# Performance work log

Hardware: AMD Instinct MI355X
Metric: run time of the kernel (lower is better)

## Reference

```python
import jax, jax.numpy as jnp
import numpy as np

B, S, IN, HID, NH, HD, R, WIN, TK = 2, 2048, 64, 512, 8, 64, 64, 5, 16
C1, C2, C3 = 171, 171, 170  # hidden_dim split across 3 conv branches (512 = 171+171+170)


def _conv(xc, w, b, pad):
    y = jax.lax.conv_general_dilated(xc, w, window_strides=(1,), padding=[(pad, pad)],
                                     dimension_numbers=('NCH', 'OIH', 'NCH'))
    return jax.nn.relu(y + b[None, :, None])


def setup_inputs():
    key = jax.random.key(0)
    ks = jax.random.split(key, 22)
    p = lambda k, sh: jax.random.normal(k, sh, jnp.float32) * 0.05
    return {
        'x': jax.random.normal(ks[0], (B, S, IN), jnp.float32),
        'conv1_w': p(ks[1], (C1, IN, 3)), 'conv1_b': p(ks[2], (C1,)),
        'conv2_w': p(ks[3], (C2, IN, 5)), 'conv2_b': p(ks[4], (C2,)),
        'conv3_w': p(ks[5], (C3, IN, 7)), 'conv3_b': p(ks[6], (C3,)),
        'Wq': p(ks[7], (HID, HID)), 'bq': p(ks[8], (HID,)),
        'Wk': p(ks[9], (HID, HID)), 'bk': p(ks[10], (HID,)),
        'Wv': p(ks[11], (HID, HID)), 'bv': p(ks[12], (HID,)),
        'Wkp': p(ks[13], (R, HD)), 'bkp': p(ks[14], (R,)),
        'Wvp': p(ks[15], (R, HD)), 'bvp': p(ks[16], (R,)),
        'Wo': p(ks[17], (HID, HID)), 'bo': p(ks[18], (HID,)),
        'ln_g': jnp.ones((HID,), jnp.float32), 'ln_b': jnp.zeros((HID,), jnp.float32),
    }


def reference(x, conv1_w, conv1_b, conv2_w, conv2_b, conv3_w, conv3_b,
              Wq, bq, Wk, bk, Wv, bv, Wkp, bkp, Wvp, bvp, Wo, bo, ln_g, ln_b):
    # multi-scale conv front-end
    xc = x.transpose(0, 2, 1)  # [B, IN, S]
    h = jnp.concatenate([_conv(xc, conv1_w, conv1_b, 1),
                         _conv(xc, conv2_w, conv2_b, 2),
                         _conv(xc, conv3_w, conv3_b, 3)], axis=1).transpose(0, 2, 1)  # [B,S,HID]

    def heads(W_, b_):
        return (h @ W_.T + b_).reshape(B, S, NH, HD).transpose(0, 2, 1, 3)  # [B,NH,S,HD]

    Q, K, V = heads(Wq, bq), heads(Wk, bk), heads(Wv, bv)
    Kp = K @ Wkp.T + bkp  # [B,NH,S,R]
    Vp = V @ Wvp.T + bvp

    # local sliding-window attention; -inf masking reproduces the per-t boundary slicing
    hw = WIN // 2
    idx = jnp.arange(S)[:, None] + jnp.arange(-hw, hw + 1)[None, :]
    valid = (idx >= 0) & (idx < S)
    idxc = jnp.clip(idx, 0, S - 1)
    Kw = K[:, :, idxc, :]
    Vw = V[:, :, idxc, :]
    ls = jnp.einsum('bhsd,bhswd->bhsw', Q, Kw) / jnp.sqrt(jnp.float32(HD))
    ls = jnp.where(valid[None, None], ls, -jnp.inf)
    local = jnp.einsum('bhsw,bhswd->bhsd', jax.nn.softmax(ls, axis=-1), Vw)

    # top-k low-rank global attention (HD == R required by original einsum)
    gs = jnp.einsum('bhqd,bhkd->bhqk', Q, Kp) / jnp.sqrt(jnp.float32(R))  # [B,NH,S,S]
    tv, ti = jax.lax.top_k(gs, TK)
    tw = jax.nn.softmax(tv, axis=-1)  # [B,NH,S,TK]
    bi = jnp.arange(B)[:, None, None, None]
    hi = jnp.arange(NH)[None, :, None, None]
    topV = Vp[bi, hi, ti]  # [B,NH,S,TK,R]
    sp = jnp.einsum('bhqk,bhqkr->bhqr', tw, topV)
    sp = sp @ Wvp.T + bvp  # extra value_proj applied to sparse output, as in original

    out = ((local + sp) * 0.5).transpose(0, 2, 1, 3).reshape(B, S, HID)
    out = out @ Wo.T + bo
    res = out + h
    mu = res.mean(-1, keepdims=True)
    var = ((res - mu) ** 2).mean(-1, keepdims=True)
    return (res - mu) / jnp.sqrt(var + 1e-5) * ln_g + ln_b
```

## Files before the change

kernel.cpp:

```cpp
#include <hip/hip_runtime.h>
#include <hip/hip_bf16.h>

#define BB 2
#define SS 2048
#define INC 64
#define HIDN 512
#define NHH 8
#define HDD 64
#define SP 2054

typedef __attribute__((ext_vector_type(8))) short bf16x8;
typedef __attribute__((ext_vector_type(4))) float f32x4;

__device__ __forceinline__ short f2bf(float f) {
  union { __hip_bfloat16 h; short s; } u;
  u.h = __float2bfloat16(f);
  return u.s;
}
__device__ __forceinline__ float bf2f(short s) {
  return __uint_as_float(((unsigned)(unsigned short)s) << 16);
}


__global__ __launch_bounds__(256) void prep_kernel(
    const float* __restrict__ x, const float* __restrict__ w1,
    const float* __restrict__ b1, const float* __restrict__ w2,
    const float* __restrict__ b2, const float* __restrict__ w3,
    const float* __restrict__ b3, const float* __restrict__ bq,
    const float* __restrict__ bk_, const float* __restrict__ bv_,
    const float* __restrict__ Wkp, const float* __restrict__ Wvp,
    const float* __restrict__ bvp, float* __restrict__ ball,
    short* __restrict__ Wkpbf, short* __restrict__ W2bf,
    float* __restrict__ cvec, short* __restrict__ xbfp,
    short* __restrict__ Wcbf, float* __restrict__ bcat) {
  int i0 = blockIdx.x * 256 + threadIdx.x;
  int stride = gridDim.x * 256;
  for (int g = i0; g < BB * SP * 8; g += stride) {
    int row = g >> 3, c0 = (g & 7) << 3;
    int b = row / SP, pr = row - b * SP;
    int sg = pr - 3;
    bf16x8 v;
    if (sg >= 0 && sg < SS) {
      const float* src = x + ((size_t)(b * SS + sg) << 6) + c0;
      float4 f0 = *(const float4*)src;
      float4 f1 = *(const float4*)(src + 4);
      v[0] = f2bf(f0.x); v[1] = f2bf(f0.y); v[2] = f2bf(f0.z); v[3] = f2bf(f0.w);
      v[4] = f2bf(f1.x); v[5] = f2bf(f1.y); v[6] = f2bf(f1.z); v[7] = f2bf(f1.w);
    } else {
#pragma unroll
      for (int e = 0; e < 8; e++) v[e] = 0;
    }
    *(bf16x8*)(xbfp + ((size_t)row << 6) + c0) = v;
  }
  for (int g = i0; g < 28672; g += stride) {
    int c = g / 56;
    int rem = g - c * 56;
    int k = rem << 3;
    int t = k >> 6;
    int ci0 = k & 63;
    bf16x8 v;
#pragma unroll
    for (int e = 0; e < 8; e++) {
      int ci = ci0 + e;
      float val = 0.f;
      if (c < 171) {
        int kk = t - 2;
        if (kk >= 0 && kk < 3) val = w1[(c * 64 + ci) * 3 + kk];
      } else if (c < 342) {
        int kk = t - 1;
        if (kk >= 0 && kk < 5) val = w2[((c - 171) * 64 + ci) * 5 + kk];
      } else {
        val = w3[((c - 342) * 64 + ci) * 7 + t];
      }
      v[e] = f2bf(val);
    }
    size_t off = (size_t)(c >> 6) * 28672 + (size_t)(k >> 5) * 2048 +
                 (size_t)((c & 63) >> 4) * 512 +
                 ((((k & 31) >> 3) * 16 + (c & 15)) << 3);
    *(bf16x8*)(Wcbf + off) = v;
  }
  for (int idx = i0; idx < 4096; idx += stride) {
    Wkpbf[idx] = f2bf(Wkp[idx]);
    int j = idx >> 6, d = idx & 63;
    float s = 0.f;
#pragma unroll 8
    for (int i = 0; i < 64; i++) s += Wvp[j * 64 + i] * Wvp[i * 64 + d];
    W2bf[idx] = f2bf(s);
  }
  if (i0 < 1536) {
    float v;
    if (i0 < 512)       v = bq[i0];
    else if (i0 < 1024) v = bk_[i0 - 512];
    else                v = bv_[i0 - 1024];
    ball[i0] = v;
  }
  if (i0 < 512) {
    float v;
    if (i0 < 171)      v = b1[i0];
    else if (i0 < 342) v = b2[i0 - 171];
    else               v = b3[i0 - 342];
    bcat[i0] = v;
  }
  if (i0 < 64) {
    float s = bvp[i0];
#pragma unroll 8
    for (int i = 0; i < 64; i++) s += bvp[i] * Wvp[i0 * 64 + i];
    cvec[i0] = s;
  }
}

__global__ __launch_bounds__(256, 4) void gemm_conv_fused(
    const short* __restrict__ xbfp, const short* __restrict__ Wcbf,
    const float* __restrict__ bcat, short* __restrict__ hbf,
    short* __restrict__ hAf, const float* __restrict__ Wq,
    const float* __restrict__ Wk_, const float* __restrict__ Wv_,
    const float* __restrict__ Wo, short* __restrict__ Wallbf,
    short* __restrict__ Wobf) {
  int blk = blockIdx.x;
  int tid = threadIdx.x;
  if (blk >= 256) {
    int i0 = (blk - 256) * 256 + tid;
    if (i0 < 98304) {
      int n = i0 >> 6;
      int k = (i0 & 63) << 3;
      const float* src;
      if (n < 512)       src = Wq  + (size_t)n * 512 + k;
      else if (n < 1024) src = Wk_ + (size_t)(n - 512) * 512 + k;
      else               src = Wv_ + (size_t)(n - 1024) * 512 + k;
      float4 f0 = *(const float4*)src;
      float4 f1 = *(const float4*)(src + 4);
      bf16x8 v;
      v[0] = f2bf(f0.x); v[1] = f2bf(f0.y); v[2] = f2bf(f0.z); v[3] = f2bf(f0.w);
      v[4] = f2bf(f1.x); v[5] = f2bf(f1.y); v[6] = f2bf(f1.z); v[7] = f2bf(f1.w);
      size_t off = (size_t)(n >> 6) * 32768 + (size_t)(k >> 5) * 2048 +
                   (size_t)((n & 63) >> 4) * 512 +
                   ((((k & 31) >> 3) * 16 + (n & 15)) << 3);
      *(bf16x8*)(Wallbf + off) = v;
    } else {
      int g = i0 - 98304;
      int n = g >> 6;
      int k = (g & 63) << 3;
      const float* src = Wo + (size_t)n * 512 + k;
      float4 f0 = *(const float4*)src;
      float4 f1 = *(const float4*)(src + 4);
      bf16x8 v;
      v[0] = f2bf(f0.x); v[1] = f2bf(f0.y); v[2] = f2bf(f0.z); v[3] = f2bf(f0.w);
      v[4] = f2bf(f1.x); v[5] = f2bf(f1.y); v[6] = f2bf(f1.z); v[7] = f2bf(f1.w);
      size_t off = (size_t)(n >> 6) * 32768 + (size_t)(k >> 5) * 2048 +
                   (size_t)((n & 63) >> 4) * 512 +
                   ((((k & 31) >> 3) * 16 + (n & 15)) << 3);
      *(bf16x8*)(Wobf + off) = v;
    }
    return;
  }
  int m0 = (blk >> 3) * 128;
  int n0 = (blk & 7) * 64;
  int wvv = tid >> 6, lane = tid & 63;
  int quad = lane >> 4, l16 = lane & 15;
  int mw = m0 + wvv * 32;
  int r0 = mw + l16, r1 = r0 + 16;
  int b0 = r0 >> 11, s0 = r0 & 2047;
  int b1 = r1 >> 11, s1 = r1 & 2047;
  const short* ap0 = xbfp + (size_t)(b0 * SP + s0) * 64 + quad * 8;
  const short* ap1 = xbfp + (size_t)(b1 * SP + s1) * 64 + quad * 8;
  const short* bp = Wcbf + (size_t)(n0 >> 6) * 28672 + lane * 8;
  f32x4 acc[2][4] = {};
  bf16x8 cA0 = *(const bf16x8*)ap0;
  bf16x8 cA1 = *(const bf16x8*)ap1;
  bf16x8 cB0 = *(const bf16x8*)(bp + 0 * 512);
  bf16x8 cB1 = *(const bf16x8*)(bp + 1 * 512);
  bf16x8 cB2 = *(const bf16x8*)(bp + 2 * 512);
  bf16x8 cB3 = *(const bf16x8*)(bp + 3 * 512);
#pragma unroll 2
  for (int ks = 0; ks < 14; ks++) {
    int kn = (ks + 1 < 14 ? ks + 1 : 13);
    int offa = kn * 32;
    int offb = kn * 2048;
    bf16x8 nA0 = *(const bf16x8*)(ap0 + offa);
    bf16x8 nA1 = *(const bf16x8*)(ap1 + offa);
    bf16x8 nB0 = *(const bf16x8*)(bp + offb + 0 * 512);
    bf16x8 nB1 = *(const bf16x8*)(bp + offb + 1 * 512);
    bf16x8 nB2 = *(const bf16x8*)(bp + offb + 2 * 512);
    bf16x8 nB3 = *(const bf16x8*)(bp + offb + 3 * 512);
    acc[0][0] = __builtin_amdgcn_mfma_f32_16x16x32_bf16(cA0, cB0, acc[0][0], 0, 0, 0);
    acc[1][0] = __builtin_amdgcn_mfma_f32_16x16x32_bf16(cA1, cB0, acc[1][0], 0, 0, 0);
    acc[0][1] = __builtin_amdgcn_mfma_f32_16x16x32_bf16(cA0, cB1, acc[0][1], 0, 0, 0);
    acc[1][1] = __builtin_amdgcn_mfma_f32_16x16x32_bf16(cA1, cB1, acc[1][1], 0, 0, 0);
    acc[0][2] = __builtin_amdgcn_mfma_f32_16x16x32_bf16(cA0, cB2, acc[0][2], 0, 0, 0);
    acc[1][2] = __builtin_amdgcn_mfma_f32_16x16x32_bf16(cA1, cB2, acc[1][2], 0, 0, 0);
    acc[0][3] = __builtin_amdgcn_mfma_f32_16x16x32_bf16(cA0, cB3, acc[0][3], 0, 0, 0);
    acc[1][3] = __builtin_amdgcn_mfma_f32_16x16x32_bf16(cA1, cB3, acc[1][3], 0, 0, 0);
    cA0 = nA0; cA1 = nA1;
    cB0 = nB0; cB1 = nB1; cB2 = nB2; cB3 = nB3;
  }
#pragma unroll
  for (int mt = 0; mt < 2; mt++) {
#pragma unroll
    for (int r = 0; r < 4; r++) {
      int m = mw + mt * 16 + quad * 4 + r;
      size_t abase = (size_t)(m >> 4) * 8192;
      int m15 = m & 15;
#pragma unroll
      for (int t = 0; t < 4; t++) {
        int n = n0 + t * 16 + l16;
        float v = fmaxf(acc[mt][t][r] + bcat[n], 0.f);
        short val = f2bf(v);
        hbf[(size_t)m * 512 + n] = val;
        hAf[abase + (size_t)(n >> 5) * 512 +
            ((((n & 31) >> 3) * 16 + m15) << 3) + (n & 7)] = val;
      }
    }
  }
}

__global__ __launch_bounds__(256, 4) void gemm_qkv(
    const short* __restrict__ hAf, const short* __restrict__ Wbf,
    const float* __restrict__ bias, short* __restrict__ Qh,
    short* __restrict__ Kh, short* __restrict__ Vh) {
  int m0 = blockIdx.x * 128;
  int n0 = blockIdx.y * 64;
  int tid = threadIdx.x;
  int wvv = tid >> 6, lane = tid & 63;
  int quad = lane >> 4, l16 = lane & 15;
  int mw = m0 + wvv * 32;
  const short* ap0 = hAf + (size_t)(mw >> 4) * 8192 + lane * 8;
  const short* ap1 = ap0 + 8192;
  const short* bp = Wbf + (size_t)(n0 >> 6) * 32768 + lane * 8;
  f32x4 acc[2][4] = {};
  bf16x8 cA0 = *(const bf16x8*)ap0;
  bf16x8 cA1 = *(const bf16x8*)ap1;
  bf16x8 cB0 = *(const bf16x8*)(bp + 0 * 512);
  bf16x8 cB1 = *(const bf16x8*)(bp + 1 * 512);
  bf16x8 cB2 = *(const bf16x8*)(bp + 2 * 512);
  bf16x8 cB3 = *(const bf16x8*)(bp + 3 * 512);
#pragma unroll 2
  for (int ks = 0; ks < 16; ks++) {
    int kn = (ks + 1 < 16 ? ks + 1 : 15);
    int offab = kn * 512;
    int offb = kn * 2048;
    bf16x8 nA0 = *(const bf16x8*)(ap0 + offab);
    bf16x8 nA1 = *(const bf16x8*)(ap1 + offab);
    bf16x8 nB0 = *(const bf16x8*)(bp + offb + 0 * 512);
    bf16x8 nB1 = *(const bf16x8*)(bp + offb + 1 * 512);
    bf16x8 nB2 = *(const bf16x8*)(bp + offb + 2 * 512);
    bf16x8 nB3 = *(const bf16x8*)(bp + offb + 3 * 512);
    acc[0][0] = __builtin_amdgcn_mfma_f32_16x16x32_bf16(cA0, cB0, acc[0][0], 0, 0, 0);
    acc[1][0] = __builtin_amdgcn_mfma_f32_16x16x32_bf16(cA1, cB0, acc[1][0], 0, 0, 0);
    acc[0][1] = __builtin_amdgcn_mfma_f32_16x16x32_bf16(cA0, cB1, acc[0][1], 0, 0, 0);
    acc[1][1] = __builtin_amdgcn_mfma_f32_16x16x32_bf16(cA1, cB1, acc[1][1], 0, 0, 0);
    acc[0][2] = __builtin_amdgcn_mfma_f32_16x16x32_bf16(cA0, cB2, acc[0][2], 0, 0, 0);
    acc[1][2] = __builtin_amdgcn_mfma_f32_16x16x32_bf16(cA1, cB2, acc[1][2], 0, 0, 0);
    acc[0][3] = __builtin_amdgcn_mfma_f32_16x16x32_bf16(cA0, cB3, acc[0][3], 0, 0, 0);
    acc[1][3] = __builtin_amdgcn_mfma_f32_16x16x32_bf16(cA1, cB3, acc[1][3], 0, 0, 0);
    cA0 = nA0; cA1 = nA1;
    cB0 = nB0; cB1 = nB1; cB2 = nB2; cB3 = nB3;
  }
  int which = n0 >> 9;
  int head = (n0 >> 6) & 7;
  short* dst = which == 0 ? Qh : (which == 1 ? Kh : Vh);
  float scale = which == 0 ? 0.125f : 1.0f;
#pragma unroll
  for (int mt = 0; mt < 2; mt++) {
#pragma unroll
    for (int r = 0; r < 4; r++) {
      int m = mw + mt * 16 + quad * 4 + r;
      int bb = m >> 11, s = m & 2047;
      size_t rowoff = ((size_t)(bb * 8 + head) * 2048 + s) * 64;
#pragma unroll
      for (int t = 0; t < 4; t++) {
        int hd = t * 16 + l16;
        float v = acc[mt][t][r] + bias[n0 + hd];
        dst[rowoff + hd] = f2bf(v * scale);
      }
    }
  }
}

__global__ __launch_bounds__(256, 4) void kpvp_local_kernel(
    const short* __restrict__ Kh, const short* __restrict__ Vh,
    const short* __restrict__ Wkpbf, const float* __restrict__ bkp,
    const short* __restrict__ W2bf, const float* __restrict__ cvec,
    short* __restrict__ Kfrag, float* __restrict__ Vpp,
    const short* __restrict__ Qh, float* __restrict__ ctxl) {
  int tid = threadIdx.x;
  __shared__ float Sloc[4][2][16][17];
  __shared__ float wloc[4][16][8];
  if (blockIdx.x < 256) {
    int m0 = blockIdx.x * 128;
    int wvv = tid >> 6, lane = tid & 63;
    int quad = lane >> 4, l16 = lane & 15;
    int mw = m0 + wvv * 32;
    {
      const short* ap0 = Kh + (size_t)(mw + l16) * 64 + quad * 8;
      const short* ap1 = ap0 + 16 * 64;
      const short* bp = Wkpbf + l16 * 64 + quad * 8;
      bf16x8 A00 = *(const bf16x8*)ap0, A01 = *(const bf16x8*)(ap0 + 32);
      bf16x8 A10 = *(const bf16x8*)ap1, A11 = *(const bf16x8*)(ap1 + 32);
      f32x4 acc[2][4] = {};
#pragma unroll
      for (int t = 0; t < 4; t++) {
        bf16x8 B0 = *(const bf16x8*)(bp + t * 16 * 64);
        bf16x8 B1 = *(const bf16x8*)(bp + t * 16 * 64 + 32);
        acc[0][t] = __builtin_amdgcn_mfma_f32_16x16x32_bf16(A00, B0, acc[0][t], 0, 0, 0);
        acc[0][t] = __builtin_amdgcn_mfma_f32_16x16x32_bf16(A01, B1, acc[0][t], 0, 0, 0);
        acc[1][t] = __builtin_amdgcn_mfma_f32_16x16x32_bf16(A10, B0, acc[1][t], 0, 0, 0);
        acc[1][t] = __builtin_amdgcn_mfma_f32_16x16x32_bf16(A11, B1, acc[1][t], 0, 0, 0);
      }
#pragma unroll
      for (int mt = 0; mt < 2; mt++)
#pragma unroll
        for (int r = 0; r < 4; r++) {
          int m = mw + mt * 16 + quad * 4 + r;
          int m15 = m & 15;
          size_t gbase = (size_t)(m >> 4) * 1024;
#pragma unroll
          for (int t = 0; t < 4; t++) {
            int n = t * 16 + l16;
            short val = f2bf(acc[mt][t][r] + bkp[n]);
            Kfrag[gbase + (size_t)(n >> 5) * 512 +
                  ((((n & 31) >> 3) * 16 + m15) << 3) + (n & 7)] = val;
          }
        }
    }
    {
      const short* ap0 = Vh + (size_t)(mw + l16) * 64 + quad * 8;
      const short* ap1 = ap0 + 16 * 64;
      const short* bp = W2bf + l16 * 64 + quad * 8;
      bf16x8 A00 = *(const bf16x8*)ap0, A01 = *(const bf16x8*)(ap0 + 32);
      bf16x8 A10 = *(const bf16x8*)ap1, A11 = *(const bf16x8*)(ap1 + 32);
      f32x4 acc[2][4] = {};
#pragma unroll
      for (int t = 0; t < 4; t++) {
        bf16x8 B0 = *(const bf16x8*)(bp + t * 16 * 64);
        bf16x8 B1 = *(const bf16x8*)(bp + t * 16 * 64 + 32);
        acc[0][t] = __builtin_amdgcn_mfma_f32_16x16x32_bf16(A00, B0, acc[0][t], 0, 0, 0);
        acc[0][t] = __builtin_amdgcn_mfma_f32_16x16x32_bf16(A01, B1, acc[0][t], 0, 0, 0);
        acc[1][t] = __builtin_amdgcn_mfma_f32_16x16x32_bf16(A10, B0, acc[1][t], 0, 0, 0);
        acc[1][t] = __builtin_amdgcn_mfma_f32_16x16x32_bf16(A11, B1, acc[1][t], 0, 0, 0);
      }
#pragma unroll
      for (int mt = 0; mt < 2; mt++)
#pragma unroll
        for (int r = 0; r < 4; r++) {
          int m = mw + mt * 16 + quad * 4 + r;
#pragma unroll
          for (int t = 0; t < 4; t++) {
            int n = t * 16 + l16;
            Vpp[(size_t)m * 64 + n] = acc[mt][t][r] + cvec[n];
          }
        }
    }
    return;
  }
  int wv = tid >> 6;
  int tile = (blockIdx.x - 256) * 4 + wv;
  int bh = tile >> 7;
  int q0 = (tile & 127) * 16;
  int lane = tid & 63;
  int quad = lane >> 4, l16 = lane & 15;

  const short* qbase = Qh + (size_t)(bh * 2048 + q0 + l16) * 64 + quad * 8;
  bf16x8 a0 = *(const bf16x8*)qbase;
  bf16x8 a1 = *(const bf16x8*)(qbase + 32);

  int k0a = min(max(q0 - 2 + l16, 0), 2047);
  int k1a = min(q0 + 6 + l16, 2047);
  const short* kb0 = Kh + (size_t)(bh * 2048 + k0a) * 64 + quad * 8;
  const short* kb1 = Kh + (size_t)(bh * 2048 + k1a) * 64 + quad * 8;
  bf16x8 B00 = *(const bf16x8*)kb0;
  bf16x8 B01 = *(const bf16x8*)(kb0 + 32);
  bf16x8 B10 = *(const bf16x8*)kb1;
  bf16x8 B11 = *(const bf16x8*)(kb1 + 32);
  f32x4 C0 = {0.f, 0.f, 0.f, 0.f};
  f32x4 C1 = {0.f, 0.f, 0.f, 0.f};
  C0 = __builtin_amdgcn_mfma_f32_16x16x32_bf16(a0, B00, C0, 0, 0, 0);
  C0 = __builtin_amdgcn_mfma_f32_16x16x32_bf16(a1, B01, C0, 0, 0, 0);
  C1 = __builtin_amdgcn_mfma_f32_16x16x32_bf16(a0, B10, C1, 0, 0, 0);
  C1 = __builtin_amdgcn_mfma_f32_16x16x32_bf16(a1, B11, C1, 0, 0, 0);
#pragma unroll
  for (int r = 0; r < 4; r++) {
    Sloc[wv][0][quad * 4 + r][l16] = C0[r];
    Sloc[wv][1][quad * 4 + r][l16] = C1[r];
  }
  __builtin_amdgcn_wave_barrier();
  if (lane < 16) {
    int q = lane;
    float sc[5];
    bool ok[5];
#pragma unroll
    for (int j = 0; j < 5; j++) {
      int offq = q + j - 2;
      int sg = q0 + offq;
      ok[j] = (sg >= 0 && sg < SS);
      int t = offq <= 13 ? 0 : 1;
      int col = t ? offq - 6 : offq + 2;
      sc[j] = ok[j] ? Sloc[wv][t][q][col] : -3.0e38f;
    }
    float m = -3.0e38f;
#pragma unroll
    for (int j = 0; j < 5; j++) m = fmaxf(m, sc[j]);
    float e[5], l = 0.f;
#pragma unroll
    for (int j = 0; j < 5; j++) {
      e[j] = ok[j] ? __expf(sc[j] - m) : 0.f;
      l += e[j];
    }
    float inv = 1.f / l;
#pragma unroll
    for (int j = 0; j < 5; j++) wloc[wv][q][j] = e[j] * inv;
  }
  __builtin_amdgcn_wave_barrier();
  {
    int q = lane >> 2, jb = (lane & 3) * 16;
    int s = q0 + q;
    float acc[16] = {};
#pragma unroll
    for (int j = 0; j < 5; j++) {
      int sg = s + j - 2;
      if (sg >= 0 && sg < SS) {
        float w = wloc[wv][q][j];
        const short* vr = Vh + (size_t)(bh * 2048 + sg) * 64 + jb;
#pragma unroll
        for (int u = 0; u < 16; u += 4) {
          short4 v4 = *(const short4*)(vr + u);
          acc[u + 0] += w * bf2f(v4.x);
          acc[u + 1] += w * bf2f(v4.y);
          acc[u + 2] += w * bf2f(v4.z);
          acc[u + 3] += w * bf2f(v4.w);
        }
      }
    }
    float* orow = ctxl + (size_t)(bh * 2048 + s) * 64 + jb;
#pragma unroll
    for (int u = 0; u < 16; u += 4)
      *(float4*)(orow + u) =
          make_float4(acc[u], acc[u + 1], acc[u + 2], acc[u + 3]);
  }
}

__global__ __launch_bounds__(256, 4) void global_attn(
    const short* __restrict__ Qh, const short* __restrict__ Kfrag,
    const float* __restrict__ Vpp, const float* __restrict__ ctxl,
    short* __restrict__ ctxcb) {
  int tid = threadIdx.x;
  int wv = tid >> 6;
  int lane = tid & 63;
  int quad = lane >> 4, l16 = lane & 15;
  int tb = wv >> 1;
  int half = wv & 1;
  int p = blockIdx.x;
  int bh = (p & 7) * 2 + ((p >> 3) & 1);
  int seg = p >> 4;
  int tile = seg * 2 + tb;
  int q0 = tile * 16;

  __shared__ unsigned swl[4][16][17];
  __shared__ float twl[2][16][17];
  __shared__ int   txl[2][16][17];

  const short* qbase = Qh + (size_t)(bh * 2048 + q0 + l16) * 64 + quad * 8;
  bf16x8 a0 = *(const bf16x8*)qbase;
  bf16x8 a1 = *(const bf16x8*)(qbase + 32);

  const short* kf =
      Kfrag + (size_t)bh * (128 * 1024) + (size_t)half * (64 * 1024) + lane * 8;

  unsigned er[4][8];
#pragma unroll
  for (int a = 0; a < 4; a++)
#pragma unroll
    for (int j = 0; j < 8; j++) er[a][j] = 0u;

  auto insert8 = [&](unsigned (&e)[8], unsigned cand) {
    unsigned n0, n1, n2, n3, n4, n5, n6, n7;
    asm("v_max_u32 %0, %1, %2" : "=v"(n0) : "v"(e[0]), "v"(cand));
    asm("v_med3_u32 %0, %1, %2, %3" : "=v"(n1) : "v"(e[0]), "v"(e[1]), "v"(cand));
    asm("v_med3_u32 %0, %1, %2, %3" : "=v"(n2) : "v"(e[1]), "v"(e[2]), "v"(cand));
    asm("v_med3_u32 %0, %1, %2, %3" : "=v"(n3) : "v"(e[2]), "v"(e[3]), "v"(cand));
    asm("v_med3_u32 %0, %1, %2, %3" : "=v"(n4) : "v"(e[3]), "v"(e[4]), "v"(cand));
    asm("v_med3_u32 %0, %1, %2, %3" : "=v"(n5) : "v"(e[4]), "v"(e[5]), "v"(cand));
    asm("v_med3_u32 %0, %1, %2, %3" : "=v"(n6) : "v"(e[5]), "v"(e[6]), "v"(cand));
    asm("v_med3_u32 %0, %1, %2, %3" : "=v"(n7) : "v"(e[6]), "v"(e[7]), "v"(cand));
    e[0] = n0; e[1] = n1; e[2] = n2; e[3] = n3;
    e[4] = n4; e[5] = n5; e[6] = n6; e[7] = n7;
  };
  auto mkcand = [&](float s, int idxr) -> unsigned {
    unsigned u = __float_as_uint(s);
    u ^= ((unsigned)((int)u >> 31)) | 0x80000000u;
    return (u & 0xFFFFF800u) | (unsigned)idxr;
  };

  int idxb = 2047 - half * 1024 - l16;
#pragma unroll 4
  for (int g = 0; g < 64; g++) {
    bf16x8 B00 = *(const bf16x8*)(kf + g * 1024);
    bf16x8 B01 = *(const bf16x8*)(kf + g * 1024 + 512);
    f32x4 C0 = {0.f, 0.f, 0.f, 0.f};
    C0 = __builtin_amdgcn_mfma_f32_16x16x32_bf16(a0, B00, C0, 0, 0, 0);
    C0 = __builtin_amdgcn_mfma_f32_16x16x32_bf16(a1, B01, C0, 0, 0, 0);
    int idxr = idxb - (g << 4);
    insert8(er[0], mkcand(C0[0], idxr));
    insert8(er[1], mkcand(C0[1], idxr));
    insert8(er[2], mkcand(C0[2], idxr));
    insert8(er[3], mkcand(C0[3], idxr));
  }

  {
    unsigned sw[4] = {0u, 0u, 0u, 0u};
#pragma unroll
    for (int t = 0; t < 16; t++) {
#pragma unroll
      for (int a = 0; a < 4; a++) {
        unsigned w = er[a][0];
#pragma unroll
        for (int mm = 1; mm <= 8; mm <<= 1) {
          unsigned o = (unsigned)__shfl_xor((int)w, mm);
          w = w > o ? w : o;
        }
        bool pop = (er[a][0] == w);
#pragma unroll
        for (int j = 0; j < 7; j++) er[a][j] = pop ? er[a][j + 1] : er[a][j];
        er[a][7] = pop ? 0u : er[a][7];
        if (l16 == t) sw[a] = w;
      }
    }
#pragma unroll
    for (int a = 0; a < 4; a++) swl[wv][quad * 4 + a][l16] = sw[a];
  }
  __syncthreads();

  if (tid < 32) {
    int tb2 = tid >> 4, q = tid & 15;
    const unsigned* A = swl[tb2 * 2][q];
    const unsigned* Bv = swl[tb2 * 2 + 1][q];
    auto decode = [&](unsigned w) -> float {
      unsigned wb = w & 0xFFFFF800u;
      unsigned uu = (w & 0x80000000u) ? (wb ^ 0x80000000u) : ~wb;
      return (w == 0u) ? -1.0e30f : __uint_as_float(uu);
    };
    unsigned h0 = A[0], h1 = Bv[0];
    float mval = decode(h0 > h1 ? h0 : h1);
    float lsum = 0.f;
    float ev[16];
    int ki[16];
#pragma unroll
    for (int i = 0; i < 16; i++) {
      unsigned wa = A[i], wb2 = Bv[15 - i];
      unsigned w = wa > wb2 ? wa : wb2;
      float sv = decode(w);
      float ex = __expf(sv - mval);
      lsum += ex;
      ev[i] = ex;
      ki[i] = 2047 - (int)(w & 0x7FFu);
    }
    float inv = 1.f / lsum;
#pragma unroll
    for (int i = 0; i < 16; i++) {
      twl[tb2][q][i] = ev[i] * inv;
      txl[tb2][q][i] = ki[i];
    }
  }
  __syncthreads();

  {
    int tb2 = tid >> 7;
    int r = tid & 127;
    int q = r >> 3, d0 = (r & 7) * 8;
    int tile2 = seg * 2 + tb2;
    int q02 = tile2 * 16;
    int b = bh >> 3, hh = bh & 7;
    const float* vball = Vpp + (size_t)bh * (2048 * 64) + d0;
    float acc[8];
#pragma unroll
    for (int u = 0; u < 8; u++) acc[u] = 0.f;
#pragma unroll 4
    for (int j = 0; j < 16; j++) {
      float w = twl[tb2][q][j];
      const float* vr = vball + (size_t)txl[tb2][q][j] * 64;
      float4 v0 = *(const float4*)vr;
      float4 v1 = *(const float4*)(vr + 4);
      acc[0] += w * v0.x; acc[1] += w * v0.y;
      acc[2] += w * v0.z; acc[3] += w * v0.w;
      acc[4] += w * v1.x; acc[5] += w * v1.y;
      acc[6] += w * v1.z; acc[7] += w * v1.w;
    }
    int s = q02 + q;
    const float* lrow = ctxl + (size_t)(bh * 2048 + s) * 64 + d0;
    int M = b * 2048 + s;
    int k = hh * 64 + d0;
    size_t aoff = (size_t)(M >> 4) * 8192 + (size_t)(k >> 5) * 512 +
                  ((((k & 31) >> 3) * 16 + (M & 15)) << 3);
    float4 lv0 = *(const float4*)lrow;
    float4 lv1 = *(const float4*)(lrow + 4);
    short4 o0, o1;
    o0.x = f2bf(0.5f * (lv0.x + acc[0]));
    o0.y = f2bf(0.5f * (lv0.y + acc[1]));
    o0.z = f2bf(0.5f * (lv0.z + acc[2]));
    o0.w = f2bf(0.5f * (lv0.w + acc[3]));
    o1.x = f2bf(0.5f * (lv1.x + acc[4]));
    o1.y = f2bf(0.5f * (lv1.y + acc[5]));
    o1.z = f2bf(0.5f * (lv1.z + acc[6]));
    o1.w = f2bf(0.5f * (lv1.w + acc[7]));
    *(short4*)(ctxcb + aoff) = o0;
    *(short4*)(ctxcb + aoff + 4) = o1;
  }
}

__global__ __launch_bounds__(512, 2) void gemm_wo_ln(
    const short* __restrict__ Abf, const short* __restrict__ Wbf,
    const float* __restrict__ bo, const short* __restrict__ hbf,
    const float* __restrict__ g, const float* __restrict__ bb,
    float* __restrict__ outp) {
  int blk = blockIdx.x;
  int m0 = blk * 16;
  int tid = threadIdx.x;
  int wvv = tid >> 6, lane = tid & 63;
  int quad = lane >> 4, l16 = lane & 15;
  int n0 = wvv * 64;

  __shared__ float rowbuf[16][516];
  __shared__ float mus[16], invs[16];

  const short* ap = Abf + (size_t)blk * 8192 + lane * 8;
  const short* bp = Wbf + (size_t)wvv * 32768 + lane * 8;
  f32x4 acc[4] = {};
  bf16x8 cA = *(const bf16x8*)ap;
  bf16x8 cB0 = *(const bf16x8*)(bp + 0 * 512);
  bf16x8 cB1 = *(const bf16x8*)(bp + 1 * 512);
  bf16x8 cB2 = *(const bf16x8*)(bp + 2 * 512);
  bf16x8 cB3 = *(const bf16x8*)(bp + 3 * 512);
#pragma unroll 2
  for (int ks = 0; ks < 16; ks++) {
    int kn = (ks + 1 < 16 ? ks + 1 : 15);
    bf16x8 nA = *(const bf16x8*)(ap + kn * 512);
    bf16x8 nB0 = *(const bf16x8*)(bp + kn * 2048 + 0 * 512);
    bf16x8 nB1 = *(const bf16x8*)(bp + kn * 2048 + 1 * 512);
    bf16x8 nB2 = *(const bf16x8*)(bp + kn * 2048 + 2 * 512);
    bf16x8 nB3 = *(const bf16x8*)(bp + kn * 2048 + 3 * 512);
    acc[0] = __builtin_amdgcn_mfma_f32_16x16x32_bf16(cA, cB0, acc[0], 0, 0, 0);
    acc[1] = __builtin_amdgcn_mfma_f32_16x16x32_bf16(cA, cB1, acc[1], 0, 0, 0);
    acc[2] = __builtin_amdgcn_mfma_f32_16x16x32_bf16(cA, cB2, acc[2], 0, 0, 0);
    acc[3] = __builtin_amdgcn_mfma_f32_16x16x32_bf16(cA, cB3, acc[3], 0, 0, 0);
    cA = nA;
    cB0 = nB0; cB1 = nB1; cB2 = nB2; cB3 = nB3;
  }
#pragma unroll
  for (int r = 0; r < 4; r++) {
    int rr = quad * 4 + r;
    int m = m0 + rr;
#pragma unroll
    for (int t = 0; t < 4; t++) {
      int n = n0 + t * 16 + l16;
      rowbuf[rr][n] = acc[t][r] + bo[n] + bf2f(hbf[(size_t)m * 512 + n]);
    }
  }
  __syncthreads();
  {
    int row = tid >> 5, seg = tid & 31;
    float s = 0.f, s2 = 0.f;
#pragma unroll
    for (int u = 0; u < 16; u++) {
      float v = rowbuf[row][seg * 16 + u];
      s += v;
      s2 += v * v;
    }
#pragma unroll
    for (int off = 1; off < 32; off <<= 1) {
      s += __shfl_xor(s, off);
      s2 += __shfl_xor(s2, off);
    }
    if (seg == 0) {
      float mu = s * (1.f / 512.f);
      float var = s2 * (1.f / 512.f) - mu * mu;
      mus[row] = mu;
      invs[row] = rsqrtf(var + 1e-5f);
    }
  }
  __syncthreads();
  {
    int row = tid >> 5, seg = tid & 31;
    float mu = mus[row], inv = invs[row];
    float* orow = outp + (size_t)(m0 + row) * 512 + seg * 16;
#pragma unroll
    for (int u = 0; u < 16; u += 4) {
      int c = seg * 16 + u;
      float4 o;
      o.x = (rowbuf[row][c + 0] - mu) * inv * g[c + 0] + bb[c + 0];
      o.y = (rowbuf[row][c + 1] - mu) * inv * g[c + 1] + bb[c + 1];
      o.z = (rowbuf[row][c + 2] - mu) * inv * g[c + 2] + bb[c + 2];
      o.w = (rowbuf[row][c + 3] - mu) * inv * g[c + 3] + bb[c + 3];
      *(float4*)(orow + u) = o;
    }
  }
}

extern "C" void kernel_launch(void* const* d_in, const int* in_sizes, int n_in,
                              void* d_out, int out_size, void* d_ws,
                              size_t ws_size, hipStream_t stream) {
  const float* x   = (const float*)d_in[0];
  const float* w1  = (const float*)d_in[1];
  const float* b1  = (const float*)d_in[2];
  const float* w2  = (const float*)d_in[3];
  const float* b2  = (const float*)d_in[4];
  const float* w3  = (const float*)d_in[5];
  const float* b3  = (const float*)d_in[6];
  const float* Wq  = (const float*)d_in[7];
  const float* bq  = (const float*)d_in[8];
  const float* Wk  = (const float*)d_in[9];
  const float* bk  = (const float*)d_in[10];
  const float* Wv  = (const float*)d_in[11];
  const float* bv  = (const float*)d_in[12];
  const float* Wkp = (const float*)d_in[13];
  const float* bkp = (const float*)d_in[14];
  const float* Wvp = (const float*)d_in[15];
  const float* bvp = (const float*)d_in[16];
  const float* Wo  = (const float*)d_in[17];
  const float* bo  = (const float*)d_in[18];
  const float* lng = (const float*)d_in[19];
  const float* lnb = (const float*)d_in[20];

  float* p = (float*)d_ws;
  short* Wallbf = (short*)p;  p += 786432;
  float* ball   = p;          p += 2048;
  short* Wobf   = (short*)p;  p += 262144;
  short* Wkpbf  = (short*)p;  p += 4096;
  short* W2bf   = (short*)p;  p += 4096;
  float* cvec   = p;          p += 64;
  short* xbfp   = (short*)p;  p += 262912;
  short* Wcbf   = (short*)p;  p += 229376;
  float* bcat   = p;          p += 512;
  short* hbf    = (short*)p;  p += 1048576;
  short* hAf    = (short*)p;  p += 1048576;
  short* Qh     = (short*)p;  p += 1048576;
  short* Kh     = (short*)p;  p += 1048576;
  short* Vh     = (short*)p;  p += 1048576;
  short* Kfrag  = (short*)p;  p += 1048576;
  float* Vpp    = p;          p += 2097152;
  float* ctxl   = p;          p += 2097152;
  short* ctxcb  = (short*)p;  p += 1048576;
  float* outF   = (float*)d_out;

  prep_kernel<<<128, 256, 0, stream>>>(x, w1, b1, w2, b2, w3, b3, bq, bk, bv,
                                       Wkp, Wvp, bvp, ball, Wkpbf, W2bf, cvec,
                                       xbfp, Wcbf, bcat);
  gemm_conv_fused<<<768, 256, 0, stream>>>(xbfp, Wcbf, bcat, hbf, hAf, Wq, Wk,
                                           Wv, Wo, Wallbf, Wobf);
  {
    dim3 g(32, 24);
    gemm_qkv<<<g, 256, 0, stream>>>(hAf, Wallbf, ball, Qh, Kh, Vh);
  }
  kpvp_local_kernel<<<768, 256, 0, stream>>>(Kh, Vh, Wkpbf, bkp, W2bf, cvec,
                                             Kfrag, Vpp, Qh, ctxl);
  global_attn<<<1024, 256, 0, stream>>>(Qh, Kfrag, Vpp, ctxl, ctxcb);
  gemm_wo_ln<<<256, 512, 0, stream>>>(ctxcb, Wobf, bo, hbf, lng, lnb, outF);
}
```

Measured before the change: 210.7 us.

## Move local attention into global kernel and merge branch outputs in Wo GEMM

The local sliding-window attention now runs as extra blocks inside the global attention kernel, so the KpVp kernel only does the two small projections. Both attention branches write fp32 results in the fragment layout the Wo GEMM expects. The GEMM then averages them and converts to bf16 as it loads its A operand. This removes the dependency of global attention on the local output and overlaps the two branches. The cost is larger fp32 intermediates and extra load and convert work in the GEMM inner loop.

```diff
diff --git a/kernel.cpp b/kernel.cpp
--- a/kernel.cpp
+++ b/kernel.cpp
@@ -276,176 +276,188 @@
   }
 }
 
-__global__ __launch_bounds__(256, 4) void kpvp_local_kernel(
+__global__ __launch_bounds__(256, 4) void kpvp_kernel(
     const short* __restrict__ Kh, const short* __restrict__ Vh,
     const short* __restrict__ Wkpbf, const float* __restrict__ bkp,
     const short* __restrict__ W2bf, const float* __restrict__ cvec,
-    short* __restrict__ Kfrag, float* __restrict__ Vpp,
-    const short* __restrict__ Qh, float* __restrict__ ctxl) {
+    short* __restrict__ Kfrag, float* __restrict__ Vpp) {
   int tid = threadIdx.x;
-  __shared__ float Sloc[4][2][16][17];
-  __shared__ float wloc[4][16][8];
-  if (blockIdx.x < 256) {
-    int m0 = blockIdx.x * 128;
-    int wvv = tid >> 6, lane = tid & 63;
-    int quad = lane >> 4, l16 = lane & 15;
-    int mw = m0 + wvv * 32;
-    {
-      const short* ap0 = Kh + (size_t)(mw + l16) * 64 + quad * 8;
-      const short* ap1 = ap0 + 16 * 64;
-      const short* bp = Wkpbf + l16 * 64 + quad * 8;
-      bf16x8 A00 = *(const bf16x8*)ap0, A01 = *(const bf16x8*)(ap0 + 32);
-      bf16x8 A10 = *(const bf16x8*)ap1, A11 = *(const bf16x8*)(ap1 + 32);
-      f32x4 acc[2][4] = {};
-#pragma unroll
-      for (int t = 0; t < 4; t++) {
-        bf16x8 B0 = *(const bf16x8*)(bp + t * 16 * 64);
-        bf16x8 B1 = *(const bf16x8*)(bp + t * 16 * 64 + 32);
-        acc[0][t] = __builtin_amdgcn_mfma_f32_16x16x32_bf16(A00, B0, acc[0][t], 0, 0, 0);
-        acc[0][t] = __builtin_amdgcn_mfma_f32_16x16x32_bf16(A01, B1, acc[0][t], 0, 0, 0);
-        acc[1][t] = __builtin_amdgcn_mfma_f32_16x16x32_bf16(A10, B0, acc[1][t], 0, 0, 0);
-        acc[1][t] = __builtin_amdgcn_mfma_f32_16x16x32_bf16(A11, B1, acc[1][t], 0, 0, 0);
-      }
-#pragma unroll
-      for (int mt = 0; mt < 2; mt++)
-#pragma unroll
-        for (int r = 0; r < 4; r++) {
-          int m = mw + mt * 16 + quad * 4 + r;
-          int m15 = m & 15;
-          size_t gbase = (size_t)(m >> 4) * 1024;
-#pragma unroll
-          for (int t = 0; t < 4; t++) {
-            int n = t * 16 + l16;
-            short val = f2bf(acc[mt][t][r] + bkp[n]);
-            Kfrag[gbase + (size_t)(n >> 5) * 512 +
-                  ((((n & 31) >> 3) * 16 + m15) << 3) + (n & 7)] = val;
-          }
+  int m0 = blockIdx.x * 128;
+  int wvv = tid >> 6, lane = tid & 63;
+  int quad = lane >> 4, l16 = lane & 15;
+  int mw = m0 + wvv * 32;
+  {
+    const short* ap0 = Kh + (size_t)(mw + l16) * 64 + quad * 8;
+    const short* ap1 = ap0 + 16 * 64;
+    const short* bp = Wkpbf + l16 * 64 + quad * 8;
+    bf16x8 A00 = *(const bf16x8*)ap0, A01 = *(const bf16x8*)(ap0 + 32);
+    bf16x8 A10 = *(const bf16x8*)ap1, A11 = *(const bf16x8*)(ap1 + 32);
+    f32x4 acc[2][4] = {};
+#pragma unroll
+    for (int t = 0; t < 4; t++) {
+      bf16x8 B0 = *(const bf16x8*)(bp + t * 16 * 64);
+      bf16x8 B1 = *(const bf16x8*)(bp + t * 16 * 64 + 32);
+      acc[0][t] = __builtin_amdgcn_mfma_f32_16x16x32_bf16(A00, B0, acc[0][t], 0, 0, 0);
+      acc[0][t] = __builtin_amdgcn_mfma_f32_16x16x32_bf16(A01, B1, acc[0][t], 0, 0, 0);
+      acc[1][t] = __builtin_amdgcn_mfma_f32_16x16x32_bf16(A10, B0, acc[1][t], 0, 0, 0);
+      acc[1][t] = __builtin_amdgcn_mfma_f32_16x16x32_bf16(A11, B1, acc[1][t], 0, 0, 0);
+    }
+#pragma unroll
+    for (int mt = 0; mt < 2; mt++)
+#pragma unroll
+      for (int r = 0; r < 4; r++) {
+        int m = mw + mt * 16 + quad * 4 + r;
+        int m15 = m & 15;
+        size_t gbase = (size_t)(m >> 4) * 1024;
+#pragma unroll
+        for (int t = 0; t < 4; t++) {
+          int n = t * 16 + l16;
+          short val = f2bf(acc[mt][t][r] + bkp[n]);
+          Kfrag[gbase + (size_t)(n >> 5) * 512 +
+                ((((n & 31) >> 3) * 16 + m15) << 3) + (n & 7)] = val;
         }
-    }
-    {
-      const short* ap0 = Vh + (size_t)(mw + l16) * 64 + quad * 8;
-      const short* ap1 = ap0 + 16 * 64;
-      const short* bp = W2bf + l16 * 64 + quad * 8;
-      bf16x8 A00 = *(const bf16x8*)ap0, A01 = *(const bf16x8*)(ap0 + 32);
-      bf16x8 A10 = *(const bf16x8*)ap1, A11 = *(const bf16x8*)(ap1 + 32);
-      f32x4 acc[2][4] = {};
-#pragma unroll
-      for (int t = 0; t < 4; t++) {
-        bf16x8 B0 = *(const bf16x8*)(bp + t * 16 * 64);
-        bf16x8 B1 = *(const bf16x8*)(bp + t * 16 * 64 + 32);
-        acc[0][t] = __builtin_amdgcn_mfma_f32_16x16x32_bf16(A00, B0, acc[0][t], 0, 0, 0);
-        acc[0][t] = __builtin_amdgcn_mfma_f32_16x16x32_bf16(A01, B1, acc[0][t], 0, 0, 0);
-        acc[1][t] = __builtin_amdgcn_mfma_f32_16x16x32_bf16(A10, B0, acc[1][t], 0, 0, 0);
-        acc[1][t] = __builtin_amdgcn_mfma_f32_16x16x32_bf16(A11, B1, acc[1][t], 0, 0, 0);
-      }
-#pragma unroll
-      for (int mt = 0; mt < 2; mt++)
-#pragma unroll
-        for (int r = 0; r < 4; r++) {
-          int m = mw + mt * 16 + quad * 4 + r;
-#pragma unroll
-          for (int t = 0; t < 4; t++) {
-            int n = t * 16 + l16;
-            Vpp[(size_t)m * 64 + n] = acc[mt][t][r] + cvec[n];
-          }
+      }
+  }
+  {
+    const short* ap0 = Vh + (size_t)(mw + l16) * 64 + quad * 8;
+    const short* ap1 = ap0 + 16 * 64;
+    const short* bp = W2bf + l16 * 64 + quad * 8;
+    bf16x8 A00 = *(const bf16x8*)ap0, A01 = *(const bf16x8*)(ap0 + 32);
+    bf16x8 A10 = *(const bf16x8*)ap1, A11 = *(const bf16x8*)(ap1 + 32);
+    f32x4 acc[2][4] = {};
+#pragma unroll
+    for (int t = 0; t < 4; t++) {
+      bf16x8 B0 = *(const bf16x8*)(bp + t * 16 * 64);
+      bf16x8 B1 = *(const bf16x8*)(bp + t * 16 * 64 + 32);
+      acc[0][t] = __builtin_amdgcn_mfma_f32_16x16x32_bf16(A00, B0, acc[0][t], 0, 0, 0);
+      acc[0][t] = __builtin_amdgcn_mfma_f32_16x16x32_bf16(A01, B1, acc[0][t], 0, 0, 0);
+      acc[1][t] = __builtin_amdgcn_mfma_f32_16x16x32_bf16(A10, B0, acc[1][t], 0, 0, 0);
+      acc[1][t] = __builtin_amdgcn_mfma_f32_16x16x32_bf16(A11, B1, acc[1][t], 0, 0, 0);
+    }
+#pragma unroll
+    for (int mt = 0; mt < 2; mt++)
+#pragma unroll
+      for (int r = 0; r < 4; r++) {
+        int m = mw + mt * 16 + quad * 4 + r;
+#pragma unroll
+        for (int t = 0; t < 4; t++) {
+          int n = t * 16 + l16;
+          Vpp[(size_t)m * 64 + n] = acc[mt][t][r] + cvec[n];
         }
-    }
-    return;
-  }
-  int wv = tid >> 6;
-  int tile = (blockIdx.x - 256) * 4 + wv;
-  int bh = tile >> 7;
-  int q0 = (tile & 127) * 16;
-  int lane = tid & 63;
-  int quad = lane >> 4, l16 = lane & 15;
-
-  const short* qbase = Qh + (size_t)(bh * 2048 + q0 + l16) * 64 + quad * 8;
-  bf16x8 a0 = *(const bf16x8*)qbase;
-  bf16x8 a1 = *(const bf16x8*)(qbase + 32);
-
-  int k0a = min(max(q0 - 2 + l16, 0), 2047);
-  int k1a = min(q0 + 6 + l16, 2047);
-  const short* kb0 = Kh + (size_t)(bh * 2048 + k0a) * 64 + quad * 8;
-  const short* kb1 = Kh + (size_t)(bh * 2048 + k1a) * 64 + quad * 8;
-  bf16x8 B00 = *(const bf16x8*)kb0;
-  bf16x8 B01 = *(const bf16x8*)(kb0 + 32);
-  bf16x8 B10 = *(const bf16x8*)kb1;
-  bf16x8 B11 = *(const bf16x8*)(kb1 + 32);
-  f32x4 C0 = {0.f, 0.f, 0.f, 0.f};
-  f32x4 C1 = {0.f, 0.f, 0.f, 0.f};
-  C0 = __builtin_amdgcn_mfma_f32_16x16x32_bf16(a0, B00, C0, 0, 0, 0);
-  C0 = __builtin_amdgcn_mfma_f32_16x16x32_bf16(a1, B01, C0, 0, 0, 0);
-  C1 = __builtin_amdgcn_mfma_f32_16x16x32_bf16(a0, B10, C1, 0, 0, 0);
-  C1 = __builtin_amdgcn_mfma_f32_16x16x32_bf16(a1, B11, C1, 0, 0, 0);
-#pragma unroll
-  for (int r = 0; r < 4; r++) {
-    Sloc[wv][0][quad * 4 + r][l16] = C0[r];
-    Sloc[wv][1][quad * 4 + r][l16] = C1[r];
-  }
-  __builtin_amdgcn_wave_barrier();
-  if (lane < 16) {
-    int q = lane;
-    float sc[5];
-    bool ok[5];
-#pragma unroll
-    for (int j = 0; j < 5; j++) {
-      int offq = q + j - 2;
-      int sg = q0 + offq;
-      ok[j] = (sg >= 0 && sg < SS);
-      int t = offq <= 13 ? 0 : 1;
-      int col = t ? offq - 6 : offq + 2;
-      sc[j] = ok[j] ? Sloc[wv][t][q][col] : -3.0e38f;
-    }
-    float m = -3.0e38f;
-#pragma unroll
-    for (int j = 0; j < 5; j++) m = fmaxf(m, sc[j]);
-    float e[5], l = 0.f;
-#pragma unroll
-    for (int j = 0; j < 5; j++) {
-      e[j] = ok[j] ? __expf(sc[j] - m) : 0.f;
-      l += e[j];
-    }
-    float inv = 1.f / l;
-#pragma unroll
-    for (int j = 0; j < 5; j++) wloc[wv][q][j] = e[j] * inv;
-  }
-  __builtin_amdgcn_wave_barrier();
-  {
-    int q = lane >> 2, jb = (lane & 3) * 16;
-    int s = q0 + q;
-    float acc[16] = {};
-#pragma unroll
-    for (int j = 0; j < 5; j++) {
-      int sg = s + j - 2;
-      if (sg >= 0 && sg < SS) {
-        float w = wloc[wv][q][j];
-        const short* vr = Vh + (size_t)(bh * 2048 + sg) * 64 + jb;
-#pragma unroll
-        for (int u = 0; u < 16; u += 4) {
-          short4 v4 = *(const short4*)(vr + u);
-          acc[u + 0] += w * bf2f(v4.x);
-          acc[u + 1] += w * bf2f(v4.y);
-          acc[u + 2] += w * bf2f(v4.z);
-          acc[u + 3] += w * bf2f(v4.w);
-        }
-      }
-    }
-    float* orow = ctxl + (size_t)(bh * 2048 + s) * 64 + jb;
-#pragma unroll
-    for (int u = 0; u < 16; u += 4)
-      *(float4*)(orow + u) =
-          make_float4(acc[u], acc[u + 1], acc[u + 2], acc[u + 3]);
-  }
-}
-
-__global__ __launch_bounds__(256, 4) void global_attn(
+      }
+  }
+}
+
+__global__ __launch_bounds__(256, 4) void global_local_kernel(
     const short* __restrict__ Qh, const short* __restrict__ Kfrag,
-    const float* __restrict__ Vpp, const float* __restrict__ ctxl,
-    short* __restrict__ ctxcb) {
+    const float* __restrict__ Vpp, const short* __restrict__ Kh,
+    const short* __restrict__ Vh, float* __restrict__ spA,
+    float* __restrict__ ctxlA) {
   int tid = threadIdx.x;
   int wv = tid >> 6;
   int lane = tid & 63;
   int quad = lane >> 4, l16 = lane & 15;
+
+  __shared__ unsigned swl[4][16][17];
+  __shared__ float twl[2][16][17];
+  __shared__ int   txl[2][16][17];
+  __shared__ float Sloc[4][2][16][17];
+  __shared__ float wloc[4][16][8];
+
+  if (blockIdx.x >= 1024) {
+    int tile = (blockIdx.x - 1024) * 4 + wv;
+    int bh = tile >> 7;
+    int q0 = (tile & 127) * 16;
+
+    const short* qbase = Qh + (size_t)(bh * 2048 + q0 + l16) * 64 + quad * 8;
+    bf16x8 a0 = *(const bf16x8*)qbase;
+    bf16x8 a1 = *(const bf16x8*)(qbase + 32);
+
+    int k0a = min(max(q0 - 2 + l16, 0), 2047);
+    int k1a = min(q0 + 6 + l16, 2047);
+    const short* kb0 = Kh + (size_t)(bh * 2048 + k0a) * 64 + quad * 8;
+    const short* kb1 = Kh + (size_t)(bh * 2048 + k1a) * 64 + quad * 8;
+    bf16x8 B00 = *(const bf16x8*)kb0;
+    bf16x8 B01 = *(const bf16x8*)(kb0 + 32);
+    bf16x8 B10 = *(const bf16x8*)kb1;
+    bf16x8 B11 = *(const bf16x8*)(kb1 + 32);
+    f32x4 C0 = {0.f, 0.f, 0.f, 0.f};
+    f32x4 C1 = {0.f, 0.f, 0.f, 0.f};
+    C0 = __builtin_amdgcn_mfma_f32_16x16x32_bf16(a0, B00, C0, 0, 0, 0);
+    C0 = __builtin_amdgcn_mfma_f32_16x16x32_bf16(a1, B01, C0, 0, 0, 0);
+    C1 = __builtin_amdgcn_mfma_f32_16x16x32_bf16(a0, B10, C1, 0, 0, 0);
+    C1 = __builtin_amdgcn_mfma_f32_16x16x32_bf16(a1, B11, C1, 0, 0, 0);
+#pragma unroll
+    for (int r = 0; r < 4; r++) {
+      Sloc[wv][0][quad * 4 + r][l16] = C0[r];
+      Sloc[wv][1][quad * 4 + r][l16] = C1[r];
+    }
+    __builtin_amdgcn_wave_barrier();
+    if (lane < 16) {
+      int q = lane;
+      float sc[5];
+      bool ok[5];
+#pragma unroll
+      for (int j = 0; j < 5; j++) {
+        int offq = q + j - 2;
+        int sg = q0 + offq;
+        ok[j] = (sg >= 0 && sg < SS);
+        int t = offq <= 13 ? 0 : 1;
+        int col = t ? offq - 6 : offq + 2;
+        sc[j] = ok[j] ? Sloc[wv][t][q][col] : -3.0e38f;
+      }
+      float m = -3.0e38f;
+#pragma unroll
+      for (int j = 0; j < 5; j++) m = fmaxf(m, sc[j]);
+      float e[5], l = 0.f;
+#pragma unroll
+      for (int j = 0; j < 5; j++) {
+        e[j] = ok[j] ? __expf(sc[j] - m) : 0.f;
+        l += e[j];
+      }
+      float inv = 1.f / l;
+#pragma unroll
+      for (int j = 0; j < 5; j++) wloc[wv][q][j] = e[j] * inv;
+    }
+    __builtin_amdgcn_wave_barrier();
+    {
+      int q = lane >> 2, jb = (lane & 3) * 16;
+      int s = q0 + q;
+      float acc[16] = {};
+#pragma unroll
+      for (int j = 0; j < 5; j++) {
+        int sg = s + j - 2;
+        if (sg >= 0 && sg < SS) {
+          float w = wloc[wv][q][j];
+          const short* vr = Vh + (size_t)(bh * 2048 + sg) * 64 + jb;
+#pragma unroll
+          for (int u = 0; u < 16; u += 4) {
+            short4 v4 = *(const short4*)(vr + u);
+            acc[u + 0] += w * bf2f(v4.x);
+            acc[u + 1] += w * bf2f(v4.y);
+            acc[u + 2] += w * bf2f(v4.z);
+            acc[u + 3] += w * bf2f(v4.w);
+          }
+        }
+      }
+      int b = bh >> 3, hh = bh & 7;
+      int M = b * 2048 + s;
+      int m15 = M & 15;
+      size_t mbase = (size_t)(M >> 4) * 8192;
+#pragma unroll
+      for (int u = 0; u < 16; u += 8) {
+        int k0 = hh * 64 + jb + u;
+        size_t off = mbase + (size_t)(k0 >> 5) * 512 +
+                     ((((k0 & 31) >> 3) * 16 + m15) << 3);
+        *(float4*)(ctxlA + off) =
+            make_float4(acc[u], acc[u + 1], acc[u + 2], acc[u + 3]);
+        *(float4*)(ctxlA + off + 4) =
+            make_float4(acc[u + 4], acc[u + 5], acc[u + 6], acc[u + 7]);
+      }
+    }
+    return;
+  }
+
   int tb = wv >> 1;
   int half = wv & 1;
   int p = blockIdx.x;
@@ -453,10 +465,6 @@
   int seg = p >> 4;
   int tile = seg * 2 + tb;
   int q0 = tile * 16;
-
-  __shared__ unsigned swl[4][16][17];
-  __shared__ float twl[2][16][17];
-  __shared__ int   txl[2][16][17];
 
   const short* qbase = Qh + (size_t)(bh * 2048 + q0 + l16) * 64 + quad * 8;
   bf16x8 a0 = *(const bf16x8*)qbase;
@@ -585,32 +593,20 @@
       acc[6] += w * v1.z; acc[7] += w * v1.w;
     }
     int s = q02 + q;
-    const float* lrow = ctxl + (size_t)(bh * 2048 + s) * 64 + d0;
     int M = b * 2048 + s;
     int k = hh * 64 + d0;
     size_t aoff = (size_t)(M >> 4) * 8192 + (size_t)(k >> 5) * 512 +
                   ((((k & 31) >> 3) * 16 + (M & 15)) << 3);
-    float4 lv0 = *(const float4*)lrow;
-    float4 lv1 = *(const float4*)(lrow + 4);
-    short4 o0, o1;
-    o0.x = f2bf(0.5f * (lv0.x + acc[0]));
-    o0.y = f2bf(0.5f * (lv0.y + acc[1]));
-    o0.z = f2bf(0.5f * (lv0.z + acc[2]));
-    o0.w = f2bf(0.5f * (lv0.w + acc[3]));
-    o1.x = f2bf(0.5f * (lv1.x + acc[4]));
-    o1.y = f2bf(0.5f * (lv1.y + acc[5]));
-    o1.z = f2bf(0.5f * (lv1.z + acc[6]));
-    o1.w = f2bf(0.5f * (lv1.w + acc[7]));
-    *(short4*)(ctxcb + aoff) = o0;
-    *(short4*)(ctxcb + aoff + 4) = o1;
+    *(float4*)(spA + aoff) = make_float4(acc[0], acc[1], acc[2], acc[3]);
+    *(float4*)(spA + aoff + 4) = make_float4(acc[4], acc[5], acc[6], acc[7]);
   }
 }
 
 __global__ __launch_bounds__(512, 2) void gemm_wo_ln(
-    const short* __restrict__ Abf, const short* __restrict__ Wbf,
-    const float* __restrict__ bo, const short* __restrict__ hbf,
-    const float* __restrict__ g, const float* __restrict__ bb,
-    float* __restrict__ outp) {
+    const float* __restrict__ ctxlA, const float* __restrict__ spA,
+    const short* __restrict__ Wbf, const float* __restrict__ bo,
+    const short* __restrict__ hbf, const float* __restrict__ g,
+    const float* __restrict__ bb, float* __restrict__ outp) {
   int blk = blockIdx.x;
   int m0 = blk * 16;
   int tid = threadIdx.x;
@@ -621,10 +617,29 @@
   __shared__ float rowbuf[16][516];
   __shared__ float mus[16], invs[16];
 
-  const short* ap = Abf + (size_t)blk * 8192 + lane * 8;
+  const float* lA = ctxlA + (size_t)blk * 8192 + lane * 8;
+  const float* sA = spA + (size_t)blk * 8192 + lane * 8;
   const short* bp = Wbf + (size_t)wvv * 32768 + lane * 8;
+
+  auto loadA = [&](int koff) -> bf16x8 {
+    float4 l0 = *(const float4*)(lA + koff);
+    float4 l1 = *(const float4*)(lA + koff + 4);
+    float4 s0 = *(const float4*)(sA + koff);
+    float4 s1 = *(const float4*)(sA + koff + 4);
+    bf16x8 v;
+    v[0] = f2bf(0.5f * (l0.x + s0.x));
+    v[1] = f2bf(0.5f * (l0.y + s0.y));
+    v[2] = f2bf(0.5f * (l0.z + s0.z));
+    v[3] = f2bf(0.5f * (l0.w + s0.w));
+    v[4] = f2bf(0.5f * (l1.x + s1.x));
+    v[5] = f2bf(0.5f * (l1.y + s1.y));
+    v[6] = f2bf(0.5f * (l1.z + s1.z));
+    v[7] = f2bf(0.5f * (l1.w + s1.w));
+    return v;
+  };
+
   f32x4 acc[4] = {};
-  bf16x8 cA = *(const bf16x8*)ap;
+  bf16x8 cA = loadA(0);
   bf16x8 cB0 = *(const bf16x8*)(bp + 0 * 512);
   bf16x8 cB1 = *(const bf16x8*)(bp + 1 * 512);
   bf16x8 cB2 = *(const bf16x8*)(bp + 2 * 512);
@@ -632,7 +647,7 @@
 #pragma unroll 2
   for (int ks = 0; ks < 16; ks++) {
     int kn = (ks + 1 < 16 ? ks + 1 : 15);
-    bf16x8 nA = *(const bf16x8*)(ap + kn * 512);
+    bf16x8 nA = loadA(kn * 512);
     bf16x8 nB0 = *(const bf16x8*)(bp + kn * 2048 + 0 * 512);
     bf16x8 nB1 = *(const bf16x8*)(bp + kn * 2048 + 1 * 512);
     bf16x8 nB2 = *(const bf16x8*)(bp + kn * 2048 + 2 * 512);
@@ -736,8 +751,8 @@
   short* Vh     = (short*)p;  p += 1048576;
   short* Kfrag  = (short*)p;  p += 1048576;
   float* Vpp    = p;          p += 2097152;
-  float* ctxl   = p;          p += 2097152;
-  short* ctxcb  = (short*)p;  p += 1048576;
+  float* ctxlA  = p;          p += 2097152;
+  float* spA    = p;          p += 2097152;
   float* outF   = (float*)d_out;
 
   prep_kernel<<<128, 256, 0, stream>>>(x, w1, b1, w2, b2, w3, b3, bq, bk, bv,
@@ -749,8 +764,10 @@
     dim3 g(32, 24);
     gemm_qkv<<<g, 256, 0, stream>>>(hAf, Wallbf, ball, Qh, Kh, Vh);
   }
-  kpvp_local_kernel<<<768, 256, 0, stream>>>(Kh, Vh, Wkpbf, bkp, W2bf, cvec,
-                                             Kfrag, Vpp, Qh, ctxl);
-  global_attn<<<1024, 256, 0, stream>>>(Qh, Kfrag, Vpp, ctxl, ctxcb);
-  gemm_wo_ln<<<256, 512, 0, stream>>>(ctxcb, Wobf, bo, hbf, lng, lnb, outF);
-}
+  kpvp_kernel<<<256, 256, 0, stream>>>(Kh, Vh, Wkpbf, bkp, W2bf, cvec, Kfrag,
+                                       Vpp);
+  global_local_kernel<<<1536, 256, 0, stream>>>(Qh, Kfrag, Vpp, Kh, Vh, spA,
+                                                ctxlA);
+  gemm_wo_ln<<<256, 512, 0, stream>>>(ctxlA, spA, Wobf, bo, hbf, lng, lnb,
+                                      outF);
+}
```

After: 212.4 us. Within noise of the previous version (+0.8%).
